# Performance work log

Measured on AMD Instinct MI355X. Metric: run time of the kernel, lower is better.

The kernel has to match this reference:

```python
import jax, jax.numpy as jnp
import numpy as np

N, C, H, W = 8, 256, 100, 252
TOPK_RATIO = 0.1
CLUSTER_RATIO = 0.125
KNN_K = 10


def setup_inputs() -> dict:
    key = jax.random.key(0)
    ks = jax.random.split(key, 4)
    x = jax.random.normal(ks[0], (N, C, H, W), jnp.float32)
    w1 = jax.random.normal(ks[1], (C, C), jnp.float32) * (1.0 / np.sqrt(C))
    b1 = jnp.zeros((C,), jnp.float32)
    w2 = jax.random.normal(ks[2], (C,), jnp.float32) * (1.0 / np.sqrt(C))
    b2 = jnp.zeros((1,), jnp.float32)
    dis_priority = jnp.ones((N, H, W), jnp.float32)
    record_len = jnp.array([4, 4], dtype=jnp.int32)
    return {"x": x, "w1": w1, "b1": b1, "w2": w2, "b2": b2,
            "dis_priority": dis_priority, "record_len": record_len}


def _layernorm(t, eps=1e-5):
    mu = jnp.mean(t, -1, keepdims=True)
    var = jnp.var(t, -1, keepdims=True)
    return (t - mu) / jnp.sqrt(var + eps)


def reference(x, w1, b1, w2, b2, dis_priority, record_len):
    HW = H * W
    S = int(HW * TOPK_RATIO)                       # sampled tokens per CAV
    K = max(int(np.ceil(S * CLUSTER_RATIO)), 1)    # DPC-KNN cluster count

    xf = x.reshape(N, C, HW)
    # SortSampler: 2layer-fc-256 score net (1x1 convs == per-pixel MLP)
    h1 = jax.nn.relu(jnp.einsum('nch,dc->ndh', xf, w1) + b1[None, :, None])
    score = jax.nn.sigmoid(jnp.einsum('nch,c->nh', h1, w2) + b2)   # [N,HW]
    score = score * dis_priority.reshape(N, HW)

    conf_topk, topk_idx = jax.lax.top_k(score, S)  # descending-sort top-k
    tokens = jnp.take_along_axis(xf, topk_idx[:, None, :], axis=2)  # [N,C,S]
    tokens = _layernorm(tokens.transpose(0, 2, 1))                  # [N,S,C]
    tokens = tokens * conf_topk[..., None]

    # --- cluster_dpc_knn (TCFormer-style DPC-KNN) ---
    sq = jnp.sum(tokens * tokens, -1)
    d2 = sq[:, :, None] + sq[:, None, :] - 2.0 * jnp.einsum('bsc,btc->bst', tokens, tokens)
    dist = jnp.sqrt(jnp.maximum(d2, 1e-12)) / np.sqrt(C)            # [N,S,S]
    neg_near, _ = jax.lax.top_k(-dist, KNN_K)                       # k nearest
    density = jnp.exp(-jnp.mean(neg_near * neg_near, -1))
    density = density + jax.random.uniform(jax.random.key(1), density.shape) * 1e-6
    mask = density[:, None, :] > density[:, :, None]
    dist_max = dist.max(axis=(1, 2), keepdims=True)
    parent_dist = jnp.where(mask, dist, dist_max).min(-1)           # [N,S]
    cscore = parent_dist * density
    _, index_down = jax.lax.top_k(cscore, K)                        # [N,K]
    dist_c = jnp.take_along_axis(dist, index_down[:, :, None], axis=1)  # [N,K,S]
    idx_cluster = jnp.argmin(dist_c, axis=1)                        # [N,S]
    bidx = jnp.arange(N)[:, None]
    idx_cluster = idx_cluster.at[bidx, index_down].set(jnp.arange(K)[None, :])

    # --- merge_tokens: confidence-weighted average per cluster ---
    flat_idx = (idx_cluster + jnp.arange(N)[:, None] * K).reshape(-1)
    wgt = conf_topk.reshape(-1)
    all_w = jax.ops.segment_sum(wgt, flat_idx, num_segments=N * K) + 1e-6
    norm_w = (wgt / all_w[flat_idx])[:, None]
    merged = jax.ops.segment_sum(tokens.reshape(-1, C) * norm_w, flat_idx,
                                 num_segments=N * K).reshape(N, K, C)

    # index_points: broadcast cluster token back to its members
    src = jnp.take_along_axis(merged, idx_cluster[..., None], axis=1)  # [N,S,C]

    # scatter sampled tokens into dense spatial grid
    out = jnp.zeros((N, C, HW), x.dtype)
    out = out.at[bidx, :, topk_idx].set(src)       # [N,S] adv idx -> [N,S,C]

    # ego CAV (first in each record group) keeps full-resolution features
    starts = jnp.concatenate([jnp.zeros((1,), jnp.int32),
                              jnp.cumsum(record_len)[:-1].astype(jnp.int32)])
    is_ego = jnp.zeros((N,), bool).at[starts].set(True)
    out = jnp.where(is_ego[:, None, None], xf, out)
    return out.reshape(N, C, H, W)
```

## Files before the change

### kernel.cpp

```cpp
#include <hip/hip_runtime.h>
#include <cstdio>
#include <cstdint>

#define NN  8
#define CCH 256
#define HWP 25200
#define SS  2520
#define KCL 315
#define KNN 10

__device__ __forceinline__ unsigned fmap(float f) {
  unsigned u = __float_as_uint(f);
  return (u & 0x80000000u) ? ~u : (u | 0x80000000u);
}

__global__ __launch_bounds__(256) void k_w1t(const float* __restrict__ w1, float* __restrict__ w1T) {
  __shared__ float tile[32][33];
  const int bx = blockIdx.x * 32, by = blockIdx.y * 32;
  const int tx = threadIdx.x, ty = threadIdx.y;
  for (int r = 0; r < 32; r += 8)
    tile[ty + r][tx] = w1[(by + ty + r) * CCH + bx + tx];
  __syncthreads();
  for (int r = 0; r < 32; r += 8)
    w1T[(bx + ty + r) * CCH + by + tx] = tile[tx][ty + r];
}

__global__ __launch_bounds__(256) void k_score(
    const float* __restrict__ x, const float* __restrict__ w1T,
    const float* __restrict__ b1, const float* __restrict__ w2,
    const float* __restrict__ b2, const float* __restrict__ pri,
    float* __restrict__ scores)
{
  __shared__ float Wl[16 * 256];
  __shared__ float Xl[16 * 64];
  __shared__ float red[64 * 33];
  const int n = blockIdx.y, p0 = blockIdx.x * 64, tid = threadIdx.x;
  const int dt = tid & 31, pt = tid >> 5;
  float acc[8][8];
#pragma unroll
  for (int i = 0; i < 8; ++i)
#pragma unroll
    for (int j = 0; j < 8; ++j) acc[i][j] = 0.f;

  for (int c0 = 0; c0 < CCH; c0 += 16) {
    {
      const float4* src = (const float4*)(w1T + (size_t)c0 * CCH);
      float4* dst = (float4*)Wl;
#pragma unroll
      for (int i = 0; i < 4; ++i) dst[tid + 256 * i] = src[tid + 256 * i];
    }
    {
      int kk = tid >> 4, q = tid & 15;
      int gp = p0 + 4 * q; if (gp > HWP - 4) gp = HWP - 4;
      *(float4*)&Xl[kk * 64 + 4 * q] = *(const float4*)&x[(size_t)(n * CCH + c0 + kk) * HWP + gp];
    }
    __syncthreads();
#pragma unroll
    for (int kk = 0; kk < 16; ++kk) {
      const float4 w0 = *(const float4*)&Wl[kk * 256 + 4 * dt];
      const float4 w1v = *(const float4*)&Wl[kk * 256 + 128 + 4 * dt];
      const float4 x0 = *(const float4*)&Xl[kk * 64 + 4 * pt];
      const float4 x1 = *(const float4*)&Xl[kk * 64 + 32 + 4 * pt];
      const float a[8] = {w0.x, w0.y, w0.z, w0.w, w1v.x, w1v.y, w1v.z, w1v.w};
      const float b[8] = {x0.x, x0.y, x0.z, x0.w, x1.x, x1.y, x1.z, x1.w};
#pragma unroll
      for (int di = 0; di < 8; ++di)
#pragma unroll
        for (int pj = 0; pj < 8; ++pj) acc[di][pj] += a[di] * b[pj];
    }
    __syncthreads();
  }
  float part[8];
#pragma unroll
  for (int pj = 0; pj < 8; ++pj) part[pj] = 0.f;
#pragma unroll
  for (int di = 0; di < 8; ++di) {
    int d = (di < 4) ? (4 * dt + di) : (128 + 4 * dt + di - 4);
    float bb = b1[d], wv = w2[d];
#pragma unroll
    for (int pj = 0; pj < 8; ++pj) {
      float h = acc[di][pj] + bb; h = h > 0.f ? h : 0.f;
      part[pj] += h * wv;
    }
  }
#pragma unroll
  for (int pj = 0; pj < 8; ++pj) {
    int px = (pj < 4) ? (4 * pt + pj) : (32 + 4 * pt + pj - 4);
    red[px * 33 + dt] = part[pj];
  }
  __syncthreads();
  if (tid < 64) {
    float s = b2[0];
#pragma unroll
    for (int g = 0; g < 32; ++g) s += red[tid * 33 + g];
    float sc = 1.f / (1.f + expf(-s));
    int p = p0 + tid;
    if (p < HWP) scores[n * HWP + p] = sc * pri[n * HWP + p];
  }
}

__global__ __launch_bounds__(1024) void k_topk_sample(
    const float* __restrict__ scores, int* __restrict__ topk_idx, float* __restrict__ conf)
{
  extern __shared__ float sc_lds[];
  __shared__ unsigned hist[256];
  __shared__ int wcnt[16], woff[16];
  __shared__ int sh_base, sh_tbase, sh_ngt;
  __shared__ unsigned sh_rank, sh_chosen;
  const int n = blockIdx.x, tid = threadIdx.x;
  const int lane = tid & 63, w = tid >> 6;

  {
    const float4* src = (const float4*)(scores + (size_t)n * HWP);
    float4* dst = (float4*)sc_lds;
    for (int i = tid; i < HWP / 4; i += 1024) dst[i] = src[i];
  }
  if (tid == 0) { sh_rank = SS; sh_ngt = 0; sh_base = 0; sh_tbase = 0; }
  __syncthreads();

  unsigned prefix = 0, pmask = 0;
  for (int shift = 24; shift >= 0; shift -= 8) {
    if (tid < 256) hist[tid] = 0;
    __syncthreads();
    for (int e = tid; e < HWP; e += 1024) {
      unsigned u = fmap(sc_lds[e]);
      if ((u & pmask) == prefix) atomicAdd(&hist[(u >> shift) & 255u], 1u);
    }
    __syncthreads();
    if (tid == 0) {
      unsigned r = sh_rank, chosen = 0;
      for (int b = 255; b >= 0; --b) {
        unsigned cb = hist[b];
        if (cb < r) r -= cb; else { chosen = (unsigned)b; break; }
      }
      sh_rank = r; sh_chosen = chosen;
    }
    __syncthreads();
    prefix |= sh_chosen << shift;
    pmask  |= 0xFFu << shift;
    __syncthreads();
  }
  const unsigned uT = prefix;

  {
    int myg = 0;
    for (int e = tid; e < HWP; e += 1024) myg += (fmap(sc_lds[e]) > uT);
#pragma unroll
    for (int o = 32; o > 0; o >>= 1) myg += __shfl_down(myg, o);
    if (lane == 0) atomicAdd(&sh_ngt, myg);
  }
  __syncthreads();
  const int T = SS - sh_ngt;

  for (int c0 = 0; c0 < HWP; c0 += 1024) {
    const int e = c0 + tid;
    const bool valid = e < HWP;
    const float s = valid ? sc_lds[e] : 0.f;
    const unsigned u = valid ? fmap(s) : 0u;
    const bool tie = valid && (u == uT);
    const bool gt  = valid && (u > uT);
    unsigned long long mt = __ballot(tie);
    if (lane == 0) wcnt[w] = __popcll(mt);
    __syncthreads();
    if (tid == 0) {
      int run = sh_tbase;
      for (int q = 0; q < 16; ++q) { woff[q] = run; run += wcnt[q]; }
      sh_tbase = run;
    }
    __syncthreads();
    const int trank = woff[w] + __popcll(mt & ((1ULL << lane) - 1ULL));
    const bool sel = gt || (tie && trank < T);
    unsigned long long ms = __ballot(sel);
    if (lane == 0) wcnt[w] = __popcll(ms);
    __syncthreads();
    if (tid == 0) {
      int run = sh_base;
      for (int q = 0; q < 16; ++q) { woff[q] = run; run += wcnt[q]; }
      sh_base = run;
    }
    __syncthreads();
    if (sel) {
      int pos = woff[w] + __popcll(ms & ((1ULL << lane) - 1ULL));
      topk_idx[n * SS + pos] = e;
      conf[n * SS + pos] = s;
    }
    __syncthreads();
  }
}

__device__ __forceinline__ float block_sum256(float v, float* scratch) {
#pragma unroll
  for (int o = 32; o > 0; o >>= 1) v += __shfl_down(v, o);
  int wid = threadIdx.x >> 6, lane = threadIdx.x & 63;
  if (lane == 0) scratch[wid] = v;
  __syncthreads();
  float r = scratch[0] + scratch[1] + scratch[2] + scratch[3];
  __syncthreads();
  return r;
}

__global__ __launch_bounds__(256) void k_gather_ln(
    const float* __restrict__ x, const int* __restrict__ topk_idx,
    const float* __restrict__ conf, float* __restrict__ tokens, float* __restrict__ sq)
{
  __shared__ float scratch[4];
  const int t = blockIdx.x, n = blockIdx.y, c = threadIdx.x;
  const int p = topk_idx[n * SS + t];
  float v = x[(size_t)(n * CCH + c) * HWP + p];
  float mu = block_sum256(v, scratch) * (1.f / CCH);
  float d = v - mu;
  float var = block_sum256(d * d, scratch) * (1.f / CCH);
  float inv = 1.f / sqrtf(var + 1e-5f);
  float tok = d * inv * conf[n * SS + t];
  tokens[(size_t)(n * SS + t) * CCH + c] = tok;
  float s2 = block_sum256(tok * tok, scratch);
  if (c == 0) sq[n * SS + t] = s2;
}

__global__ __launch_bounds__(256) void k_ttrans(
    const float* __restrict__ tokens, float* __restrict__ tokensT)
{
  __shared__ float tile[64][68];
  const int n = blockIdx.z, t0 = blockIdx.x * 64, cc0 = blockIdx.y * 64;
  const int tid = threadIdx.x;
  for (int l = tid; l < 1024; l += 256) {
    int tr = l >> 4, q = l & 15;
    int gt = t0 + tr;
    float4 v = {0.f, 0.f, 0.f, 0.f};
    if (gt < SS) v = *(const float4*)&tokens[(size_t)(n * SS + gt) * CCH + cc0 + 4 * q];
    *(float4*)&tile[tr][4 * q] = v;
  }
  __syncthreads();
  for (int l = tid; l < 1024; l += 256) {
    int cr = l >> 4, q = l & 15;
    int gt = t0 + 4 * q;
    if (gt <= SS - 4) {
      float4 v;
      v.x = tile[4 * q + 0][cr]; v.y = tile[4 * q + 1][cr];
      v.z = tile[4 * q + 2][cr]; v.w = tile[4 * q + 3][cr];
      *(float4*)&tokensT[(size_t)(n * CCH + cc0 + cr) * SS + gt] = v;
    }
  }
}

__global__ __launch_bounds__(256) void k_gram(
    const float* __restrict__ tokensT, const float* __restrict__ sq,
    float* __restrict__ d2, int* __restrict__ d2max)
{
  const int bi = blockIdx.y, bj = blockIdx.x, n = blockIdx.z;
  if (bj < bi) return;
  __shared__ float Al[16 * 128], Bl[16 * 128];
  __shared__ float redm[256];
  const int i0 = bi * 128, j0 = bj * 128, tid = threadIdx.x;
  const int ti = tid & 15, tj = tid >> 4;
  float acc[8][8];
#pragma unroll
  for (int i = 0; i < 8; ++i)
#pragma unroll
    for (int j = 0; j < 8; ++j) acc[i][j] = 0.f;

  for (int c0 = 0; c0 < CCH; c0 += 16) {
#pragma unroll
    for (int l0 = 0; l0 < 2; ++l0) {
      int l = threadIdx.x + 256 * l0;
      int kk = l >> 5, q = l & 31;
      size_t srow = (size_t)(n * CCH + c0 + kk) * SS;
      float4 z = {0.f, 0.f, 0.f, 0.f};
      int gi = i0 + 4 * q;
      *(float4*)&Al[kk * 128 + 4 * q] = (gi <= SS - 4) ? *(const float4*)&tokensT[srow + gi] : z;
      int gj = j0 + 4 * q;
      *(float4*)&Bl[kk * 128 + 4 * q] = (gj <= SS - 4) ? *(const float4*)&tokensT[srow + gj] : z;
    }
    __syncthreads();
#pragma unroll
    for (int kk = 0; kk < 16; ++kk) {
      const float4 a0 = *(const float4*)&Al[kk * 128 + 4 * ti];
      const float4 a1 = *(const float4*)&Al[kk * 128 + 64 + 4 * ti];
      const float4 b0 = *(const float4*)&Bl[kk * 128 + 4 * tj];
      const float4 b1 = *(const float4*)&Bl[kk * 128 + 64 + 4 * tj];
      const float a[8] = {a0.x, a0.y, a0.z, a0.w, a1.x, a1.y, a1.z, a1.w};
      const float b[8] = {b0.x, b0.y, b0.z, b0.w, b1.x, b1.y, b1.z, b1.w};
#pragma unroll
      for (int ii = 0; ii < 8; ++ii)
#pragma unroll
        for (int jj = 0; jj < 8; ++jj) acc[ii][jj] += a[ii] * b[jj];
    }
    __syncthreads();
  }
  int gi[8], gj[8];
  float sqi[8], sqj[8];
#pragma unroll
  for (int ii = 0; ii < 8; ++ii) {
    gi[ii] = i0 + ((ii < 4) ? (4 * ti + ii) : (64 + 4 * ti + ii - 4));
    sqi[ii] = (gi[ii] < SS) ? sq[n * SS + gi[ii]] : 0.f;
    gj[ii] = j0 + ((ii < 4) ? (4 * tj + ii) : (64 + 4 * tj + ii - 4));
    sqj[ii] = (gj[ii] < SS) ? sq[n * SS + gj[ii]] : 0.f;
  }
  float outv[8][8];
  float mx = -3e38f;
#pragma unroll
  for (int ii = 0; ii < 8; ++ii)
#pragma unroll
    for (int jj = 0; jj < 8; ++jj) {
      float o = sqi[ii] + sqj[jj] - 2.f * acc[ii][jj];
      outv[ii][jj] = o;
      if (gi[ii] < SS && gj[jj] < SS) mx = fmaxf(mx, o);
    }
#pragma unroll
  for (int ii = 0; ii < 8; ++ii) {
    if (gi[ii] < SS) {
      size_t row = (size_t)(n * SS + gi[ii]) * SS;
      int jb0 = j0 + 4 * tj;
      float4 o0 = {outv[ii][0], outv[ii][1], outv[ii][2], outv[ii][3]};
      *(float4*)&d2[row + jb0] = o0;
      int jb1 = j0 + 64 + 4 * tj;
      if (jb1 < SS) {
        float4 o1 = {outv[ii][4], outv[ii][5], outv[ii][6], outv[ii][7]};
        *(float4*)&d2[row + jb1] = o1;
      }
    }
  }
  if (bi != bj) {
#pragma unroll
    for (int jj = 0; jj < 8; ++jj) {
      if (gj[jj] < SS) {
        size_t row = (size_t)(n * SS + gj[jj]) * SS;
        int ib0 = i0 + 4 * ti;
        float4 m0 = {outv[0][jj], outv[1][jj], outv[2][jj], outv[3][jj]};
        *(float4*)&d2[row + ib0] = m0;
        int ib1 = i0 + 64 + 4 * ti;
        if (ib1 < SS) {
          float4 m1 = {outv[4][jj], outv[5][jj], outv[6][jj], outv[7][jj]};
          *(float4*)&d2[row + ib1] = m1;
        }
      }
    }
  }
  redm[tid] = mx; __syncthreads();
  for (int s = 128; s > 0; s >>= 1) {
    if (tid < s) redm[tid] = fmaxf(redm[tid], redm[tid + s]);
    __syncthreads();
  }
  if (tid == 0) atomicMax(&d2max[n], __float_as_int(redm[0]));
}

__global__ __launch_bounds__(256) void k_knn(
    const float* __restrict__ d2, float* __restrict__ density)
{
  const int n = blockIdx.y;
  const int w = threadIdx.x >> 6, lane = threadIdx.x & 63;
  const int i = blockIdx.x * 4 + w;
  const float* dr = &d2[(size_t)(n * SS + i) * SS];
  float s[KNN];
#pragma unroll
  for (int k = 0; k < KNN; ++k) s[k] = 3e38f;
  for (int e = lane; e < SS; e += 64) {
    float t = dr[e];
#pragma unroll
    for (int k = 0; k < KNN; ++k) {
      float lo = fminf(s[k], t);
      t = fmaxf(s[k], t);
      s[k] = lo;
    }
  }
  float sum = 0.f;
  for (int r = 0; r < KNN; ++r) {
    float m = s[0];
#pragma unroll
    for (int o = 32; o > 0; o >>= 1) m = fminf(m, __shfl_xor(m, o));
    unsigned long long msk = __ballot(s[0] == m);
    int first = __ffsll(msk) - 1;
    if (lane == first) {
#pragma unroll
      for (int k = 0; k < KNN - 1; ++k) s[k] = s[k + 1];
      s[KNN - 1] = 3e38f;
    }
    sum += fmaxf(m, 1e-12f);
  }
  if (lane == 0) density[n * SS + i] = expf(-sum * (1.f / (KNN * CCH)));
}

__global__ __launch_bounds__(256) void k_parent(
    const float* __restrict__ d2, const float* __restrict__ density,
    const int* __restrict__ d2max, float* __restrict__ cscore)
{
  __shared__ float swv[4];
  const int i = blockIdx.x, n = blockIdx.y, tid = threadIdx.x;
  const float di = density[n * SS + i];
  const float* dr = &d2[(size_t)(n * SS + i) * SS];
  float m = 3e38f;
  for (int e = tid; e < SS; e += 256) {
    float dj = density[n * SS + e];
    float v = dr[e];
    if (dj > di && v < m) m = v;
  }
#pragma unroll
  for (int o = 32; o > 0; o >>= 1) m = fminf(m, __shfl_down(m, o));
  int wid = tid >> 6, lane = tid & 63;
  if (lane == 0) swv[wid] = m;
  __syncthreads();
  if (tid == 0) {
    float mm = fminf(fminf(swv[0], swv[1]), fminf(swv[2], swv[3]));
    mm = fminf(mm, __int_as_float(d2max[n]));
    float pd = sqrtf(fmaxf(mm, 1e-12f)) * 0.0625f;
    cscore[n * SS + i] = pd * di;
  }
}

__global__ __launch_bounds__(1024) void k_topk_centers(
    const float* __restrict__ cscore, int* __restrict__ index_down)
{
  __shared__ float cs_lds[SS];
  __shared__ unsigned hist[256];
  __shared__ int wcnt[16], woff[16];
  __shared__ int sh_base, sh_tbase, sh_ngt;
  __shared__ unsigned sh_rank, sh_chosen;
  const int n = blockIdx.x, tid = threadIdx.x;
  const int lane = tid & 63, w = tid >> 6;

  for (int e = tid; e < SS; e += 1024) cs_lds[e] = cscore[n * SS + e];
  if (tid == 0) { sh_rank = KCL; sh_ngt = 0; sh_base = 0; sh_tbase = 0; }
  __syncthreads();

  unsigned prefix = 0, pmask = 0;
  for (int shift = 24; shift >= 0; shift -= 8) {
    if (tid < 256) hist[tid] = 0;
    __syncthreads();
    for (int e = tid; e < SS; e += 1024) {
      unsigned u = fmap(cs_lds[e]);
      if ((u & pmask) == prefix) atomicAdd(&hist[(u >> shift) & 255u], 1u);
    }
    __syncthreads();
    if (tid == 0) {
      unsigned r = sh_rank, chosen = 0;
      for (int b = 255; b >= 0; --b) {
        unsigned cb = hist[b];
        if (cb < r) r -= cb; else { chosen = (unsigned)b; break; }
      }
      sh_rank = r; sh_chosen = chosen;
    }
    __syncthreads();
    prefix |= sh_chosen << shift;
    pmask  |= 0xFFu << shift;
    __syncthreads();
  }
  const unsigned uT = prefix;

  {
    int myg = 0;
    for (int e = tid; e < SS; e += 1024) myg += (fmap(cs_lds[e]) > uT);
#pragma unroll
    for (int o = 32; o > 0; o >>= 1) myg += __shfl_down(myg, o);
    if (lane == 0) atomicAdd(&sh_ngt, myg);
  }
  __syncthreads();
  const int T = KCL - sh_ngt;

  for (int c0 = 0; c0 < SS; c0 += 1024) {
    const int e = c0 + tid;
    const bool valid = e < SS;
    const unsigned u = valid ? fmap(cs_lds[e]) : 0u;
    const bool tie = valid && (u == uT);
    const bool gt  = valid && (u > uT);
    unsigned long long mt = __ballot(tie);
    if (lane == 0) wcnt[w] = __popcll(mt);
    __syncthreads();
    if (tid == 0) {
      int run = sh_tbase;
      for (int q = 0; q < 16; ++q) { woff[q] = run; run += wcnt[q]; }
      sh_tbase = run;
    }
    __syncthreads();
    const int trank = woff[w] + __popcll(mt & ((1ULL << lane) - 1ULL));
    const bool sel = gt || (tie && trank < T);
    unsigned long long ms = __ballot(sel);
    if (lane == 0) wcnt[w] = __popcll(ms);
    __syncthreads();
    if (tid == 0) {
      int run = sh_base;
      for (int q = 0; q < 16; ++q) { woff[q] = run; run += wcnt[q]; }
      sh_base = run;
    }
    __syncthreads();
    if (sel) {
      int pos = woff[w] + __popcll(ms & ((1ULL << lane) - 1ULL));
      index_down[n * KCL + pos] = e;
    }
    __syncthreads();
  }
}

__global__ __launch_bounds__(256) void k_assign(
    const float* __restrict__ d2, const int* __restrict__ index_down,
    const float* __restrict__ conf, const int* __restrict__ topk_idx,
    int* __restrict__ idx_cluster, float* __restrict__ all_w, int* __restrict__ kmap)
{
  const int n = blockIdx.y;
  const int i = blockIdx.x * 256 + threadIdx.x;
  if (i >= SS) return;
  float best = 3e38f; int bk = 0, forced = -1;
  for (int k = 0; k < KCL; ++k) {
    int r = index_down[n * KCL + k];
    if (r == i) forced = k;
    float v = d2[(size_t)(n * SS + r) * SS + i];
    if (v < best) { best = v; bk = k; }
  }
  if (forced >= 0) bk = forced;
  idx_cluster[n * SS + i] = bk;
  atomicAdd(&all_w[n * KCL + bk], conf[n * SS + i]);
  kmap[n * HWP + topk_idx[n * SS + i]] = bk;
}

__global__ __launch_bounds__(256) void k_merge(
    const int* __restrict__ idx_cluster, const float* __restrict__ conf,
    const float* __restrict__ all_w, const float* __restrict__ tokens, float* __restrict__ merged)
{
  const int t = blockIdx.x, n = blockIdx.y, c = threadIdx.x;
  const int k = idx_cluster[n * SS + t];
  const float w = conf[n * SS + t] / (all_w[n * KCL + k] + 1e-6f);
  atomicAdd(&merged[(size_t)(n * KCL + k) * CCH + c],
            tokens[(size_t)(n * SS + t) * CCH + c] * w);
}

__global__ __launch_bounds__(256) void k_output(
    const float* __restrict__ x, const float* __restrict__ merged,
    const int* __restrict__ kmap, const int* __restrict__ rec, int R,
    float* __restrict__ out)
{
  const int n = blockIdx.z, c = blockIdx.y;
  const int p4 = blockIdx.x * 256 + threadIdx.x;
  if (p4 >= HWP / 4) return;
  bool ego = false;
  {
    int acc = 0;
    for (int r = 0; r < R; ++r) { if (acc == n) ego = true; acc += rec[r]; }
  }
  const size_t base = (size_t)(n * CCH + c) * HWP + 4 * p4;
  float4 v;
  if (ego) {
    v = *(const float4*)&x[base];
  } else {
    int4 k4 = *(const int4*)&kmap[n * HWP + 4 * p4];
    const float* mb = &merged[(size_t)n * KCL * CCH + c];
    v.x = (k4.x >= 0) ? mb[(size_t)k4.x * CCH] : 0.f;
    v.y = (k4.y >= 0) ? mb[(size_t)k4.y * CCH] : 0.f;
    v.z = (k4.z >= 0) ? mb[(size_t)k4.z * CCH] : 0.f;
    v.w = (k4.w >= 0) ? mb[(size_t)k4.w * CCH] : 0.f;
  }
  *(float4*)&out[base] = v;
}

extern "C" void kernel_launch(void* const* d_in, const int* in_sizes, int n_in,
                              void* d_out, int out_size, void* d_ws, size_t ws_size,
                              hipStream_t stream)
{
  const float* x   = (const float*)d_in[0];
  const float* w1  = (const float*)d_in[1];
  const float* b1  = (const float*)d_in[2];
  const float* w2  = (const float*)d_in[3];
  const float* b2  = (const float*)d_in[4];
  const float* pri = (const float*)d_in[5];
  const int*   rec = (const int*)d_in[6];
  const int R = in_sizes[6];
  float* out = (float*)d_out;

  char* ws = (char*)d_ws;
  size_t off = 0;
  auto alloc = [&](size_t bytes) -> char* {
    char* p = ws + off;
    off = (off + bytes + 255) & ~(size_t)255;
    return p;
  };
  float* scores      = (float*)alloc(sizeof(float) * NN * HWP);
  int*   topk_idx    = (int*)  alloc(sizeof(int)   * NN * SS);
  float* conf        = (float*)alloc(sizeof(float) * NN * SS);
  float* tokens      = (float*)alloc(sizeof(float) * (size_t)NN * SS * CCH);
  float* tokensT     = (float*)alloc(sizeof(float) * (size_t)NN * CCH * SS);
  float* w1T         = (float*)alloc(sizeof(float) * CCH * CCH);
  float* sq          = (float*)alloc(sizeof(float) * NN * SS);
  float* density     = (float*)alloc(sizeof(float) * NN * SS);
  float* cscore      = (float*)alloc(sizeof(float) * NN * SS);
  int*   d2max       = (int*)  alloc(sizeof(int)   * NN);
  int*   index_down  = (int*)  alloc(sizeof(int)   * NN * KCL);
  int*   idx_cluster = (int*)  alloc(sizeof(int)   * NN * SS);
  float* all_w       = (float*)alloc(sizeof(float) * NN * KCL);
  float* merged      = (float*)alloc(sizeof(float) * (size_t)NN * KCL * CCH);
  int*   kmap        = (int*)  alloc(sizeof(int)   * NN * HWP);
  float* d2          = (float*)alloc(sizeof(float) * (size_t)NN * SS * SS);
  if (off > ws_size)
    fprintf(stderr, "ERMVP kernel: workspace too small: need %zu, have %zu\n", off, ws_size);

  hipMemsetAsync(d2max, 0, sizeof(int) * NN, stream);
  hipMemsetAsync(all_w, 0, sizeof(float) * NN * KCL, stream);
  hipMemsetAsync(merged, 0, sizeof(float) * (size_t)NN * KCL * CCH, stream);
  hipMemsetAsync(kmap, 0xFF, sizeof(int) * NN * HWP, stream);

  k_w1t<<<dim3(8, 8), dim3(32, 8), 0, stream>>>(w1, w1T);
  k_score<<<dim3((HWP + 63) / 64, NN), 256, 0, stream>>>(x, w1T, b1, w2, b2, pri, scores);
  k_topk_sample<<<NN, 1024, sizeof(float) * HWP, stream>>>(scores, topk_idx, conf);
  k_gather_ln<<<dim3(SS, NN), 256, 0, stream>>>(x, topk_idx, conf, tokens, sq);
  k_ttrans<<<dim3((SS + 63) / 64, CCH / 64, NN), 256, 0, stream>>>(tokens, tokensT);
  k_gram<<<dim3(20, 20, NN), 256, 0, stream>>>(tokensT, sq, d2, d2max);
  k_knn<<<dim3(SS / 4, NN), 256, 0, stream>>>(d2, density);
  k_parent<<<dim3(SS, NN), 256, 0, stream>>>(d2, density, d2max, cscore);
  k_topk_centers<<<NN, 1024, 0, stream>>>(cscore, index_down);
  k_assign<<<dim3((SS + 255) / 256, NN), 256, 0, stream>>>(d2, index_down, conf, topk_idx,
                                                           idx_cluster, all_w, kmap);
  k_merge<<<dim3(SS, NN), 256, 0, stream>>>(idx_cluster, conf, all_w, tokens, merged);
  k_output<<<dim3((HWP / 4 + 255) / 256, CCH, NN), 256, 0, stream>>>(x, merged, kmap, rec, R, out);
}
```

Before: 1.211 ms.

## Replace atomic scatter merge with per-cluster gather reduction

```diff
diff --git a/kernel.cpp b/kernel.cpp
--- a/kernel.cpp
+++ b/kernel.cpp
@@ -492,8 +492,8 @@
 
 __global__ __launch_bounds__(256) void k_assign(
     const float* __restrict__ d2, const int* __restrict__ index_down,
-    const float* __restrict__ conf, const int* __restrict__ topk_idx,
-    int* __restrict__ idx_cluster, float* __restrict__ all_w, int* __restrict__ kmap)
+    const int* __restrict__ topk_idx,
+    int* __restrict__ idx_cluster, int* __restrict__ kmap)
 {
   const int n = blockIdx.y;
   const int i = blockIdx.x * 256 + threadIdx.x;
@@ -507,19 +507,37 @@
   }
   if (forced >= 0) bk = forced;
   idx_cluster[n * SS + i] = bk;
-  atomicAdd(&all_w[n * KCL + bk], conf[n * SS + i]);
   kmap[n * HWP + topk_idx[n * SS + i]] = bk;
 }
 
 __global__ __launch_bounds__(256) void k_merge(
     const int* __restrict__ idx_cluster, const float* __restrict__ conf,
-    const float* __restrict__ all_w, const float* __restrict__ tokens, float* __restrict__ merged)
-{
-  const int t = blockIdx.x, n = blockIdx.y, c = threadIdx.x;
-  const int k = idx_cluster[n * SS + t];
-  const float w = conf[n * SS + t] / (all_w[n * KCL + k] + 1e-6f);
-  atomicAdd(&merged[(size_t)(n * KCL + k) * CCH + c],
-            tokens[(size_t)(n * SS + t) * CCH + c] * w);
+    const float* __restrict__ tokens, float* __restrict__ merged)
+{
+  __shared__ int mlist[SS];
+  __shared__ float scratch[4];
+  __shared__ int sh_cnt;
+  const int k = blockIdx.x, n = blockIdx.y, tid = threadIdx.x;
+  if (tid == 0) sh_cnt = 0;
+  __syncthreads();
+  for (int t = tid; t < SS; t += 256) {
+    if (idx_cluster[n * SS + t] == k) {
+      int s = atomicAdd(&sh_cnt, 1);
+      mlist[s] = t;
+    }
+  }
+  __syncthreads();
+  const int cnt = sh_cnt;
+  float ws = 0.f;
+  for (int i = tid; i < cnt; i += 256) ws += conf[n * SS + mlist[i]];
+  ws = block_sum256(ws, scratch);
+  const float inv = 1.f / (ws + 1e-6f);
+  float acc = 0.f;
+  for (int i = 0; i < cnt; ++i) {
+    const int t = mlist[i];
+    acc += tokens[(size_t)(n * SS + t) * CCH + tid] * conf[n * SS + t];
+  }
+  merged[(size_t)(n * KCL + k) * CCH + tid] = acc * inv;
 }
 
 __global__ __launch_bounds__(256) void k_output(
@@ -583,7 +601,6 @@
   int*   d2max       = (int*)  alloc(sizeof(int)   * NN);
   int*   index_down  = (int*)  alloc(sizeof(int)   * NN * KCL);
   int*   idx_cluster = (int*)  alloc(sizeof(int)   * NN * SS);
-  float* all_w       = (float*)alloc(sizeof(float) * NN * KCL);
   float* merged      = (float*)alloc(sizeof(float) * (size_t)NN * KCL * CCH);
   int*   kmap        = (int*)  alloc(sizeof(int)   * NN * HWP);
   float* d2          = (float*)alloc(sizeof(float) * (size_t)NN * SS * SS);
@@ -591,8 +608,6 @@
     fprintf(stderr, "ERMVP kernel: workspace too small: need %zu, have %zu\n", off, ws_size);
 
   hipMemsetAsync(d2max, 0, sizeof(int) * NN, stream);
-  hipMemsetAsync(all_w, 0, sizeof(float) * NN * KCL, stream);
-  hipMemsetAsync(merged, 0, sizeof(float) * (size_t)NN * KCL * CCH, stream);
   hipMemsetAsync(kmap, 0xFF, sizeof(int) * NN * HWP, stream);
 
   k_w1t<<<dim3(8, 8), dim3(32, 8), 0, stream>>>(w1, w1T);
@@ -604,8 +619,8 @@
   k_knn<<<dim3(SS / 4, NN), 256, 0, stream>>>(d2, density);
   k_parent<<<dim3(SS, NN), 256, 0, stream>>>(d2, density, d2max, cscore);
   k_topk_centers<<<NN, 1024, 0, stream>>>(cscore, index_down);
-  k_assign<<<dim3((SS + 255) / 256, NN), 256, 0, stream>>>(d2, index_down, conf, topk_idx,
-                                                           idx_cluster, all_w, kmap);
-  k_merge<<<dim3(SS, NN), 256, 0, stream>>>(idx_cluster, conf, all_w, tokens, merged);
+  k_assign<<<dim3((SS + 255) / 256, NN), 256, 0, stream>>>(d2, index_down, topk_idx,
+                                                           idx_cluster, kmap);
+  k_merge<<<dim3(KCL, NN), 256, 0, stream>>>(idx_cluster, conf, tokens, merged);
   k_output<<<dim3((HWP / 4 + 255) / 256, CCH, NN), 256, 0, stream>>>(x, merged, kmap, rec, R, out);
 }
```

Result: no change. 1.222 ms (+0.9%).
